# Optimization experiments

Measured on AMD Instinct MI355X. Metric: run time of the kernel, lower is better.

The kernel has to match this reference:

```python
import jax, jax.numpy as jnp
import numpy as np

B, S, D, H = 2, 2048, 1024, 16  # batch, seq, d_model, num_heads
DH = D // H


def setup_inputs() -> dict:
    key = jax.random.key(0)
    ks = jax.random.split(key, 11)
    sc = 1.0 / np.sqrt(D)
    return {
        "q": jax.random.normal(ks[0], (B, S, D), jnp.float32),
        "k": jax.random.normal(ks[1], (B, S, D), jnp.float32),
        "v": jax.random.normal(ks[2], (B, S, D), jnp.float32),
        "wq": jax.random.normal(ks[3], (D, D), jnp.float32) * sc,
        "bq": jax.random.normal(ks[4], (D,), jnp.float32) * 0.01,
        "wk": jax.random.normal(ks[5], (D, D), jnp.float32) * sc,
        "bk": jax.random.normal(ks[6], (D,), jnp.float32) * 0.01,
        "wv": jax.random.normal(ks[7], (D, D), jnp.float32) * sc,
        "bv": jax.random.normal(ks[8], (D,), jnp.float32) * 0.01,
        "wo": jax.random.normal(ks[9], (D, D), jnp.float32) * sc,
        "bo": jax.random.normal(ks[10], (D,), jnp.float32) * 0.01,
    }


def reference(q, k, v, wq, bq, wk, bk, wv, bv, wo, bo):
    # projections: [B,S,D]
    query = q @ wq + bq
    key_ = k @ wk + bk
    value = v @ wv + bv
    # split heads: [B,H,S,DH]
    def split(x):
        return jnp.transpose(x.reshape(B, S, H, DH), (0, 2, 1, 3))
    query, key_, value = split(query), split(key_), split(value)
    # NOTE: original module applies NO 1/sqrt(d_k) scaling
    scores = jnp.einsum("bhqd,bhkd->bhqk", query, key_)
    attn = jax.nn.softmax(scores, axis=-1)
    data = jnp.einsum("bhqk,bhkd->bhqd", attn, value)  # [B,H,S,DH]
    # faithful to original bug: transpose(0,1) then view(B,S,-1)
    data = jnp.swapaxes(data, 0, 1).reshape(B, S, D)
    return data @ wo + bo
```

## Files before the change

### kernel.cpp

```cpp
#include <hip/hip_runtime.h>

typedef _Float16 f16;
typedef _Float16 f16x8 __attribute__((ext_vector_type(8)));
typedef _Float16 f16x4 __attribute__((ext_vector_type(4)));
typedef float    f32x4 __attribute__((ext_vector_type(4)));

static constexpr int BATCH = 2, SEQ = 2048, DMODEL = 1024, HEADS = 16, DHEAD = 64;
static constexpr int MTOK = BATCH * SEQ;
static constexpr float LOG2E = 1.44269504088896f;

#define GLOBAL_LOAD_LDS16(gptr, lptr)                                              \
  __builtin_amdgcn_global_load_lds(                                                \
      (const __attribute__((address_space(1))) void*)(gptr),                       \
      (__attribute__((address_space(3))) void*)(lptr), 16, 0, 0)

#define MFMA16(a, b, c) __builtin_amdgcn_mfma_f32_16x16x32_f16((a), (b), (c), 0, 0, 0)

__device__ __forceinline__ float fexp2(float x) {
  float r;
  asm volatile("v_exp_f32 %0, %1" : "=v"(r) : "v"(x));
  return r;
}

__device__ __forceinline__ int imgAB(int mr, int kr) {
  int pr = mr >> 1;
  int jj = ((mr & 1) << 2) | (kr >> 3);
  int j = jj ^ (pr & 7);
  return pr * 64 + j * 8 + (kr & 7);
}
__device__ __forceinline__ int imgK(int sr, int dh) {
  return sr * 64 + (((dh >> 3) ^ (sr & 7)) << 3) + (dh & 7);
}

__global__ __launch_bounds__(256) void cast_kernel(const float* __restrict__ src,
                                                   f16* __restrict__ dst) {
  int c = blockIdx.x * 256 + threadIdx.x;
  int blk = c >> 8, cb = c & 255;
  int pr = cb >> 3, j = cb & 7;
  int jj = j ^ (pr & 7);
  int mr = (pr << 1) | (jj >> 2);
  int kr = (jj & 3) << 3;
  int m = (blk >> 5) * 64 + mr;
  int k = (blk & 31) * 32 + kr;
  const float* s = src + (size_t)m * DMODEL + k;
  f32x4 a = *(const f32x4*)s, b = *(const f32x4*)(s + 4);
  f16x8 o;
  o[0] = (f16)a[0]; o[1] = (f16)a[1]; o[2] = (f16)a[2]; o[3] = (f16)a[3];
  o[4] = (f16)b[0]; o[5] = (f16)b[1]; o[6] = (f16)b[2]; o[7] = (f16)b[3];
  *(f16x8*)(dst + (size_t)c * 8) = o;
}

__global__ __launch_bounds__(256) void transw_kernel(
    const float* __restrict__ w0, const float* __restrict__ w1,
    const float* __restrict__ w2, const float* __restrict__ w3,
    f16* __restrict__ Wimg) {
  const int z = blockIdx.z;
  const float* w = z == 0 ? w0 : z == 1 ? w1 : z == 2 ? w2 : w3;
  f16* t = Wimg + (size_t)z * DMODEL * DMODEL;
  __shared__ f16 lt[64][72];
  const int k0 = blockIdx.x * 64, n0 = blockIdx.y * 64;
  const int r = threadIdx.x >> 2, c0 = (threadIdx.x & 3) * 16;
  const float* src = w + (size_t)(k0 + r) * DMODEL + n0 + c0;
#pragma unroll
  for (int jx = 0; jx < 16; jx += 4) {
    f32x4 x = *(const f32x4*)(src + jx);
    lt[c0 + jx + 0][r] = (f16)x[0];
    lt[c0 + jx + 1][r] = (f16)x[1];
    lt[c0 + jx + 2][r] = (f16)x[2];
    lt[c0 + jx + 3][r] = (f16)x[3];
  }
  __syncthreads();
  const int n = n0 + r;
#pragma unroll
  for (int cw = 0; cw < 2; cw++) {
    int k = k0 + c0 + cw * 8;
    int blk = ((n >> 6) << 5) | (k >> 5);
    int off = blk * 2048 + imgAB(n & 63, k & 31);
    f16x8 v;
#pragma unroll
    for (int e = 0; e < 8; e++) v[e] = lt[r][c0 + cw * 8 + e];
    *(f16x8*)(t + off) = v;
  }
}

__global__ __launch_bounds__(256) void proj_kernel(
    const f16* __restrict__ Ximg, const f16* __restrict__ Wimg,
    const float* __restrict__ bq, const float* __restrict__ bk,
    const float* __restrict__ bv, f16* __restrict__ Qp, f16* __restrict__ Kp,
    f16* __restrict__ Vt, int zbase, size_t aStride) {
  __shared__ f16 As[4096];
  __shared__ f16 Bs[4096];
  const int z = zbase + blockIdx.z;
  const f16* A = Ximg + (size_t)blockIdx.z * aStride;
  const f16* Bw = Wimg + (size_t)z * DMODEL * DMODEL;
  int lin = blockIdx.x + (blockIdx.y << 3);
  int swz = ((lin & 7) << 5) + (lin >> 3);
  const int n0 = (swz & 7) * 128, m0 = (swz >> 3) * 128;
  const int tid = threadIdx.x, w = tid >> 6, l = tid & 63, q = l & 15, g = l >> 4;
  const int wr = w >> 1, wc = w & 1;
  const int KT = DMODEL >> 5;
  int aoff[4], boff[4];
#pragma unroll
  for (int mi = 0; mi < 4; mi++) {
    int mr = wr * 64 + mi * 16 + q;
    aoff[mi] = ((mr >> 6) << 11) + imgAB(mr & 63, g * 8);
  }
#pragma unroll
  for (int ni = 0; ni < 4; ni++) {
    int nr = wc * 64 + ni * 16 + q;
    boff[ni] = ((nr >> 6) << 11) + imgAB(nr & 63, g * 8);
  }
  f32x4 acc[4][4] = {};
  for (int t = 0; t < KT; t++) {
#pragma unroll
    for (int i = 0; i < 2; i++) {
      int c = w * 2 + i;
      GLOBAL_LOAD_LDS16(A + (size_t)(((m0 >> 6) + (c >> 2)) * KT + t) * 2048 + (c & 3) * 512 + l * 8,
                        (char*)&As[c * 512]);
      GLOBAL_LOAD_LDS16(Bw + (size_t)(((n0 >> 6) + (c >> 2)) * KT + t) * 2048 + (c & 3) * 512 + l * 8,
                        (char*)&Bs[c * 512]);
    }
    __syncthreads();
    f16x8 af[4], bf[4];
#pragma unroll
    for (int mi = 0; mi < 4; mi++) af[mi] = *(const f16x8*)&As[aoff[mi]];
#pragma unroll
    for (int ni = 0; ni < 4; ni++) bf[ni] = *(const f16x8*)&Bs[boff[ni]];
#pragma unroll
    for (int mi = 0; mi < 4; mi++)
#pragma unroll
      for (int ni = 0; ni < 4; ni++)
        acc[mi][ni] = MFMA16(af[mi], bf[ni], acc[mi][ni]);
    __syncthreads();
  }
  const float* bias = z == 0 ? bq : (z == 1 ? bk : bv);
#pragma unroll
  for (int mi = 0; mi < 4; mi++)
#pragma unroll
    for (int ni = 0; ni < 4; ni++) {
      const int col = n0 + wc * 64 + ni * 16 + q;
      const float bvl = bias[col];
      const int row0 = m0 + wr * 64 + mi * 16 + g * 4;
      if (z == 0) {
#pragma unroll
        for (int r = 0; r < 4; r++)
          Qp[(size_t)(row0 + r) * DMODEL + col] = (f16)((acc[mi][ni][r] + bvl) * LOG2E);
      } else if (z == 1) {
        const int h = col >> 6, dh = col & 63;
#pragma unroll
        for (int r = 0; r < 4; r++) {
          const int row = row0 + r, s = row & (SEQ - 1);
          Kp[(size_t)(((row >> 11) * HEADS + h) * 64 + (s >> 5)) * 2048 + imgK(s & 31, dh)] =
              (f16)(acc[mi][ni][r] + bvl);
        }
      } else {
        const int h = col >> 6, dh = col & 63;
        const int s0 = row0 & (SEQ - 1);
        f16* dst = Vt + (size_t)(((row0 >> 11) * HEADS + h) * 64 + (s0 >> 5)) * 2048 +
                   imgAB(dh, s0 & 31);
        f16x4 ov;
        ov[0] = (f16)(acc[mi][ni][0] + bvl); ov[1] = (f16)(acc[mi][ni][1] + bvl);
        ov[2] = (f16)(acc[mi][ni][2] + bvl); ov[3] = (f16)(acc[mi][ni][3] + bvl);
        *(f16x4*)dst = ov;
      }
    }
}

__global__ __launch_bounds__(256) void attn_kernel(
    const f16* __restrict__ Qp, const f16* __restrict__ Kimg,
    const f16* __restrict__ Vimg, f16* __restrict__ Simg) {
  __shared__ f16 Klds[2][2048];
  __shared__ f16 Vlds[2][2048];
  __shared__ f16 Plds[4][512];
  const int tid = threadIdx.x, w = tid >> 6, l = tid & 63, q = l & 15, g = l >> 4;
  int lin = blockIdx.x + (blockIdx.y << 5);
  int swz = ((lin & 7) << 7) + (lin >> 3);
  const int qb = swz & 31, bh = swz >> 5;
  const int b = bh >> 4, h = bh & 15;
  const int q0 = qb * 64 + w * 16;
  const f16* qrow = Qp + (size_t)(b * SEQ + q0 + q) * DMODEL + h * 64;
  const f16x8 qf0 = *(const f16x8*)(qrow + g * 8);
  const f16x8 qf1 = *(const f16x8*)(qrow + 32 + g * 8);
  const f16* kt_base = Kimg + (size_t)(bh * 64) * 2048;
  const f16* vt_base = Vimg + (size_t)(bh * 64) * 2048;
  int koff[2][2];
#pragma unroll
  for (int fn = 0; fn < 2; fn++)
#pragma unroll
    for (int hf = 0; hf < 2; hf++) koff[fn][hf] = imgK(fn * 16 + q, hf * 32 + g * 8);
  int voff[4];
#pragma unroll
  for (int fo = 0; fo < 4; fo++) voff[fo] = imgAB(fo * 16 + q, g * 8);
  const int poff = imgAB(q, g * 8);
  int pwoff[2];
  {
    const int pr = q >> 1;
#pragma unroll
    for (int fn = 0; fn < 2; fn++) {
      int jj = ((q & 1) << 2) | (fn * 2 + (g >> 1));
      pwoff[fn] = pr * 64 + ((jj ^ (pr & 7)) << 3) + (g & 1) * 4;
    }
  }
  f16* Pw = &Plds[w][0];
  float m_st = -1.0e30f, l_pt = 0.f;
  f32x4 o_acc[4] = {};

  GLOBAL_LOAD_LDS16(kt_base + w * 512 + l * 8, (char*)&Klds[0][w * 512]);
  GLOBAL_LOAD_LDS16(vt_base + w * 512 + l * 8, (char*)&Vlds[0][w * 512]);
  __syncthreads();

  for (int t = 0; t < 64; t++) {
    const int bb = t & 1;
    if (t < 63) {
      GLOBAL_LOAD_LDS16(kt_base + (size_t)(t + 1) * 2048 + w * 512 + l * 8,
                        (char*)&Klds[bb ^ 1][w * 512]);
      GLOBAL_LOAD_LDS16(vt_base + (size_t)(t + 1) * 2048 + w * 512 + l * 8,
                        (char*)&Vlds[bb ^ 1][w * 512]);
    }
    const f16* Kb = &Klds[bb][0];
    const f16* Vb = &Vlds[bb][0];
    f32x4 s0 = {}, s1 = {};
    s0 = MFMA16(*(const f16x8*)(Kb + koff[0][0]), qf0, s0);
    s0 = MFMA16(*(const f16x8*)(Kb + koff[0][1]), qf1, s0);
    s1 = MFMA16(*(const f16x8*)(Kb + koff[1][0]), qf0, s1);
    s1 = MFMA16(*(const f16x8*)(Kb + koff[1][1]), qf1, s1);
    float lm = fmaxf(fmaxf(fmaxf(s0[0], s0[1]), fmaxf(s0[2], s0[3])),
                     fmaxf(fmaxf(s1[0], s1[1]), fmaxf(s1[2], s1[3])));
    if (!__all(lm <= m_st + 8.f)) {
      float mx = lm;
      mx = fmaxf(mx, __shfl_xor(mx, 16, 64));
      mx = fmaxf(mx, __shfl_xor(mx, 32, 64));
      const float mnew = fmaxf(m_st, mx);
      const float sc = fexp2(m_st - mnew);
      m_st = mnew;
      l_pt *= sc;
#pragma unroll
      for (int fo = 0; fo < 4; fo++) {
        o_acc[fo][0] *= sc; o_acc[fo][1] *= sc;
        o_acc[fo][2] *= sc; o_acc[fo][3] *= sc;
      }
    }
    f16x4 pa, pb;
    float ts = 0.f;
#pragma unroll
    for (int r = 0; r < 4; r++) {
      float e0 = fexp2(s0[r] - m_st);
      float e1 = fexp2(s1[r] - m_st);
      ts += e0 + e1;
      pa[r] = (f16)e0;
      pb[r] = (f16)e1;
    }
    l_pt += ts;
    *(f16x4*)(Pw + pwoff[0]) = pa;
    *(f16x4*)(Pw + pwoff[1]) = pb;
    const f16x8 pf = *(const f16x8*)(Pw + poff);
#pragma unroll
    for (int fo = 0; fo < 4; fo++)
      o_acc[fo] = MFMA16(*(const f16x8*)(Vb + voff[fo]), pf, o_acc[fo]);
    __syncthreads();
  }
  float lsum = l_pt + __shfl_xor(l_pt, 16, 64);
  lsum += __shfl_xor(lsum, 32, 64);
  const float inv = 1.f / lsum;
  const int s = q0 + q;
  const int m16 = (2 * h + b) & 15, bp = h >> 3;
  const int tp = bp * SEQ + m16 * 128 + (s >> 4);
#pragma unroll
  for (int fo = 0; fo < 4; fo++) {
    const int d0 = (s & 15) * 64 + fo * 16 + g * 4;
    f16* dst = Simg + (size_t)(((tp >> 6) << 5) | (d0 >> 5)) * 2048 + imgAB(tp & 63, d0 & 31);
    f16x4 ov;
    ov[0] = (f16)(o_acc[fo][0] * inv); ov[1] = (f16)(o_acc[fo][1] * inv);
    ov[2] = (f16)(o_acc[fo][2] * inv); ov[3] = (f16)(o_acc[fo][3] * inv);
    *(f16x4*)dst = ov;
  }
}

__global__ __launch_bounds__(256) void ogemm_kernel(
    const f16* __restrict__ Aimg, const f16* __restrict__ Bimg,
    const float* __restrict__ bias, float* __restrict__ out) {
  __shared__ f16 As[4096];
  __shared__ f16 Bs[2048];
  int lin = blockIdx.x + (blockIdx.y << 4);
  int swz = ((lin & 7) << 6) + (lin >> 3);
  const int n0 = (swz & 15) * 64, m0 = (swz >> 4) * 128;
  const int tid = threadIdx.x, w = tid >> 6, l = tid & 63, q = l & 15, g = l >> 4;
  const int wr = w >> 1, wc = w & 1;
  int aoff[4], boff[2];
#pragma unroll
  for (int mi = 0; mi < 4; mi++) {
    int mr = wr * 64 + mi * 16 + q;
    aoff[mi] = ((mr >> 6) << 11) + imgAB(mr & 63, g * 8);
  }
#pragma unroll
  for (int ni = 0; ni < 2; ni++) boff[ni] = imgAB(wc * 32 + ni * 16 + q, g * 8);
  f32x4 acc[4][2] = {};
  for (int t = 0; t < 32; t++) {
#pragma unroll
    for (int i = 0; i < 2; i++) {
      int c = w * 2 + i;
      GLOBAL_LOAD_LDS16(Aimg + (size_t)(((m0 >> 6) + (c >> 2)) * 32 + t) * 2048 + (c & 3) * 512 + l * 8,
                        (char*)&As[c * 512]);
    }
    GLOBAL_LOAD_LDS16(Bimg + ((size_t)(n0 >> 6) * 32 + t) * 2048 + w * 512 + l * 8,
                      (char*)&Bs[w * 512]);
    __syncthreads();
    f16x8 af[4], bf[2];
#pragma unroll
    for (int mi = 0; mi < 4; mi++) af[mi] = *(const f16x8*)&As[aoff[mi]];
#pragma unroll
    for (int ni = 0; ni < 2; ni++) bf[ni] = *(const f16x8*)&Bs[boff[ni]];
#pragma unroll
    for (int mi = 0; mi < 4; mi++)
#pragma unroll
      for (int ni = 0; ni < 2; ni++)
        acc[mi][ni] = MFMA16(af[mi], bf[ni], acc[mi][ni]);
    __syncthreads();
  }
#pragma unroll
  for (int mi = 0; mi < 4; mi++)
#pragma unroll
    for (int ni = 0; ni < 2; ni++) {
      const int col = n0 + wc * 32 + ni * 16 + q;
      const float bvl = bias[col];
      const int row0 = m0 + wr * 64 + mi * 16 + g * 4;
#pragma unroll
      for (int r = 0; r < 4; r++)
        out[(size_t)(row0 + r) * DMODEL + col] = acc[mi][ni][r] + bvl;
    }
}

extern "C" void kernel_launch(void* const* d_in, const int* in_sizes, int n_in,
                              void* d_out, int out_size, void* d_ws, size_t ws_size,
                              hipStream_t stream) {
  const float* q  = (const float*)d_in[0];
  const float* k  = (const float*)d_in[1];
  const float* v  = (const float*)d_in[2];
  const float* wq = (const float*)d_in[3];
  const float* bq = (const float*)d_in[4];
  const float* wk = (const float*)d_in[5];
  const float* bk = (const float*)d_in[6];
  const float* wv = (const float*)d_in[7];
  const float* bv = (const float*)d_in[8];
  const float* wo = (const float*)d_in[9];
  const float* bo = (const float*)d_in[10];

  const size_t XSZ = (size_t)MTOK * DMODEL;
  f16* ws = (f16*)d_ws;
  const bool fused = ws_size >= (56ull << 20);

  f16 *X0, *X1, *X2, *Qp, *Kp, *Vt, *Wimg, *scr;
  if (fused) {
    X0 = ws; X1 = ws + XSZ; X2 = ws + 2 * XSZ;
    Qp = ws + 3 * XSZ; Kp = ws + 4 * XSZ; Vt = ws + 5 * XSZ;
    Wimg = ws + 6 * XSZ;
    scr = X0;
  } else {
    X0 = X1 = X2 = ws;
    Qp = ws + XSZ; Kp = ws + 2 * XSZ; Vt = ws + 3 * XSZ;
    Wimg = ws + 4 * XSZ;
    scr = X0;
  }

  dim3 blk(256);
  dim3 gT(16, 16, 4);
  dim3 gC(2048);
  dim3 gA(32, 32);
  dim3 gO(16, 32);

  transw_kernel<<<gT, blk, 0, stream>>>(wq, wk, wv, wo, Wimg);

  if (fused) {
    cast_kernel<<<gC, blk, 0, stream>>>(q, X0);
    cast_kernel<<<gC, blk, 0, stream>>>(k, X1);
    cast_kernel<<<gC, blk, 0, stream>>>(v, X2);
    proj_kernel<<<dim3(8, 32, 3), blk, 0, stream>>>(X0, Wimg, bq, bk, bv, Qp, Kp, Vt, 0, XSZ);
  } else {
    cast_kernel<<<gC, blk, 0, stream>>>(q, X0);
    proj_kernel<<<dim3(8, 32, 1), blk, 0, stream>>>(X0, Wimg, bq, bk, bv, Qp, Kp, Vt, 0, 0);
    cast_kernel<<<gC, blk, 0, stream>>>(k, X0);
    proj_kernel<<<dim3(8, 32, 1), blk, 0, stream>>>(X0, Wimg, bq, bk, bv, Qp, Kp, Vt, 1, 0);
    cast_kernel<<<gC, blk, 0, stream>>>(v, X0);
    proj_kernel<<<dim3(8, 32, 1), blk, 0, stream>>>(X0, Wimg, bq, bk, bv, Qp, Kp, Vt, 2, 0);
  }

  attn_kernel<<<gA, blk, 0, stream>>>(Qp, Kp, Vt, scr);
  ogemm_kernel<<<gO, blk, 0, stream>>>(scr, Wimg + (size_t)3 * DMODEL * DMODEL, bo, (float*)d_out);
}
```

Measured before the change: 247.2 us.

## Rewrite attention as single-wave blocks with register K/V and deepen GEMM K-tiles

The attention kernel becomes one 64-thread wave per block. Each wave handles two 16-row query tiles and loads K and V fragments straight from global memory into registers, double-buffered. This drops the LDS staging and block-wide barriers, and K/V are reused across both query tiles. K and V are now stored in plain row-major and transposed layouts, and the projection and output GEMMs process 64-wide K steps per barrier, halving the sync count at the cost of larger LDS tiles. The risks are uncoalesced strided V loads and higher register pressure from holding two K/V buffers.

```diff
diff --git a/kernel.cpp b/kernel.cpp
--- a/kernel.cpp
+++ b/kernel.cpp
@@ -27,9 +27,6 @@
   int jj = ((mr & 1) << 2) | (kr >> 3);
   int j = jj ^ (pr & 7);
   return pr * 64 + j * 8 + (kr & 7);
-}
-__device__ __forceinline__ int imgK(int sr, int dh) {
-  return sr * 64 + (((dh >> 3) ^ (sr & 7)) << 3) + (dh & 7);
 }
 
 __global__ __launch_bounds__(256) void cast_kernel(const float* __restrict__ src,
@@ -88,8 +85,8 @@
     const float* __restrict__ bq, const float* __restrict__ bk,
     const float* __restrict__ bv, f16* __restrict__ Qp, f16* __restrict__ Kp,
     f16* __restrict__ Vt, int zbase, size_t aStride) {
-  __shared__ f16 As[4096];
-  __shared__ f16 Bs[4096];
+  __shared__ f16 As[8192];
+  __shared__ f16 Bs[8192];
   const int z = zbase + blockIdx.z;
   const f16* A = Ximg + (size_t)blockIdx.z * aStride;
   const f16* Bw = Wimg + (size_t)z * DMODEL * DMODEL;
@@ -98,39 +95,51 @@
   const int n0 = (swz & 7) * 128, m0 = (swz >> 3) * 128;
   const int tid = threadIdx.x, w = tid >> 6, l = tid & 63, q = l & 15, g = l >> 4;
   const int wr = w >> 1, wc = w & 1;
-  const int KT = DMODEL >> 5;
-  int aoff[4], boff[4];
+  int aoff[4][2], boff[4][2];
 #pragma unroll
   for (int mi = 0; mi < 4; mi++) {
     int mr = wr * 64 + mi * 16 + q;
-    aoff[mi] = ((mr >> 6) << 11) + imgAB(mr & 63, g * 8);
+#pragma unroll
+    for (int kb = 0; kb < 2; kb++)
+      aoff[mi][kb] = (((mr >> 6) << 1) | kb) * 2048 + imgAB(mr & 63, g * 8);
   }
 #pragma unroll
   for (int ni = 0; ni < 4; ni++) {
     int nr = wc * 64 + ni * 16 + q;
-    boff[ni] = ((nr >> 6) << 11) + imgAB(nr & 63, g * 8);
+#pragma unroll
+    for (int kb = 0; kb < 2; kb++)
+      boff[ni][kb] = (((nr >> 6) << 1) | kb) * 2048 + imgAB(nr & 63, g * 8);
   }
   f32x4 acc[4][4] = {};
-  for (int t = 0; t < KT; t++) {
-#pragma unroll
-    for (int i = 0; i < 2; i++) {
-      int c = w * 2 + i;
-      GLOBAL_LOAD_LDS16(A + (size_t)(((m0 >> 6) + (c >> 2)) * KT + t) * 2048 + (c & 3) * 512 + l * 8,
-                        (char*)&As[c * 512]);
-      GLOBAL_LOAD_LDS16(Bw + (size_t)(((n0 >> 6) + (c >> 2)) * KT + t) * 2048 + (c & 3) * 512 + l * 8,
-                        (char*)&Bs[c * 512]);
+  for (int t = 0; t < 16; t++) {
+#pragma unroll
+    for (int i = 0; i < 4; i++) {
+      int c = w * 4 + i;
+      int bi = c >> 2, part = c & 3;
+      size_t gblk = (size_t)(((m0 >> 6) + (bi >> 1)) * 32 + t * 2 + (bi & 1));
+      GLOBAL_LOAD_LDS16(A + gblk * 2048 + part * 512 + l * 8, (char*)&As[c * 512]);
+      size_t gblk2 = (size_t)(((n0 >> 6) + (bi >> 1)) * 32 + t * 2 + (bi & 1));
+      GLOBAL_LOAD_LDS16(Bw + gblk2 * 2048 + part * 512 + l * 8, (char*)&Bs[c * 512]);
     }
     __syncthreads();
-    f16x8 af[4], bf[4];
-#pragma unroll
-    for (int mi = 0; mi < 4; mi++) af[mi] = *(const f16x8*)&As[aoff[mi]];
-#pragma unroll
-    for (int ni = 0; ni < 4; ni++) bf[ni] = *(const f16x8*)&Bs[boff[ni]];
+    f16x8 af[4][2], bf[4][2];
+#pragma unroll
+    for (int mi = 0; mi < 4; mi++) {
+      af[mi][0] = *(const f16x8*)&As[aoff[mi][0]];
+      af[mi][1] = *(const f16x8*)&As[aoff[mi][1]];
+    }
+#pragma unroll
+    for (int ni = 0; ni < 4; ni++) {
+      bf[ni][0] = *(const f16x8*)&Bs[boff[ni][0]];
+      bf[ni][1] = *(const f16x8*)&Bs[boff[ni][1]];
+    }
 #pragma unroll
     for (int mi = 0; mi < 4; mi++)
 #pragma unroll
-      for (int ni = 0; ni < 4; ni++)
-        acc[mi][ni] = MFMA16(af[mi], bf[ni], acc[mi][ni]);
+      for (int ni = 0; ni < 4; ni++) {
+        acc[mi][ni] = MFMA16(af[mi][0], bf[ni][0], acc[mi][ni]);
+        acc[mi][ni] = MFMA16(af[mi][1], bf[ni][1], acc[mi][ni]);
+      }
     __syncthreads();
   }
   const float* bias = z == 0 ? bq : (z == 1 ? bk : bv);
@@ -146,18 +155,13 @@
         for (int r = 0; r < 4; r++)
           Qp[(size_t)(row0 + r) * DMODEL + col] = (f16)((acc[mi][ni][r] + bvl) * LOG2E);
       } else if (z == 1) {
-        const int h = col >> 6, dh = col & 63;
-#pragma unroll
-        for (int r = 0; r < 4; r++) {
-          const int row = row0 + r, s = row & (SEQ - 1);
-          Kp[(size_t)(((row >> 11) * HEADS + h) * 64 + (s >> 5)) * 2048 + imgK(s & 31, dh)] =
-              (f16)(acc[mi][ni][r] + bvl);
-        }
+#pragma unroll
+        for (int r = 0; r < 4; r++)
+          Kp[(size_t)(row0 + r) * DMODEL + col] = (f16)(acc[mi][ni][r] + bvl);
       } else {
         const int h = col >> 6, dh = col & 63;
-        const int s0 = row0 & (SEQ - 1);
-        f16* dst = Vt + (size_t)(((row0 >> 11) * HEADS + h) * 64 + (s0 >> 5)) * 2048 +
-                   imgAB(dh, s0 & 31);
+        const int b2 = row0 >> 11, s0 = row0 & (SEQ - 1);
+        f16* dst = Vt + ((size_t)(b2 * HEADS + h) * DHEAD + dh) * SEQ + s0;
         f16x4 ov;
         ov[0] = (f16)(acc[mi][ni][0] + bvl); ov[1] = (f16)(acc[mi][ni][1] + bvl);
         ov[2] = (f16)(acc[mi][ni][2] + bvl); ov[3] = (f16)(acc[mi][ni][3] + bvl);
@@ -166,32 +170,30 @@
     }
 }
 
-__global__ __launch_bounds__(256) void attn_kernel(
-    const f16* __restrict__ Qp, const f16* __restrict__ Kimg,
-    const f16* __restrict__ Vimg, f16* __restrict__ Simg) {
-  __shared__ f16 Klds[2][2048];
-  __shared__ f16 Vlds[2][2048];
-  __shared__ f16 Plds[4][512];
-  const int tid = threadIdx.x, w = tid >> 6, l = tid & 63, q = l & 15, g = l >> 4;
-  int lin = blockIdx.x + (blockIdx.y << 5);
-  int swz = ((lin & 7) << 7) + (lin >> 3);
-  const int qb = swz & 31, bh = swz >> 5;
+__global__ __launch_bounds__(64, 2) void attn_kernel(
+    const f16* __restrict__ Qp, const f16* __restrict__ Kp,
+    const f16* __restrict__ Vt, f16* __restrict__ Simg) {
+  __shared__ f16 Plds[1024];
+  const int l = threadIdx.x, q = l & 15, g = l >> 4;
+  const int bid = blockIdx.x;
+  const int gid = (bid & 7) * 256 + (bid >> 3);
+  const int bh = gid >> 6, qt = gid & 63;
   const int b = bh >> 4, h = bh & 15;
-  const int q0 = qb * 64 + w * 16;
-  const f16* qrow = Qp + (size_t)(b * SEQ + q0 + q) * DMODEL + h * 64;
-  const f16x8 qf0 = *(const f16x8*)(qrow + g * 8);
-  const f16x8 qf1 = *(const f16x8*)(qrow + 32 + g * 8);
-  const f16* kt_base = Kimg + (size_t)(bh * 64) * 2048;
-  const f16* vt_base = Vimg + (size_t)(bh * 64) * 2048;
-  int koff[2][2];
-#pragma unroll
-  for (int fn = 0; fn < 2; fn++)
-#pragma unroll
-    for (int hf = 0; hf < 2; hf++) koff[fn][hf] = imgK(fn * 16 + q, hf * 32 + g * 8);
-  int voff[4];
-#pragma unroll
-  for (int fo = 0; fo < 4; fo++) voff[fo] = imgAB(fo * 16 + q, g * 8);
-  const int poff = imgAB(q, g * 8);
+  const int q0 = qt * 32;
+
+  const f16* qra = Qp + (size_t)(b * SEQ + q0 + q) * DMODEL + h * 64;
+  const f16x8 qa0 = *(const f16x8*)(qra + g * 8);
+  const f16x8 qa1 = *(const f16x8*)(qra + 32 + g * 8);
+  const f16* qrb = qra + (size_t)16 * DMODEL;
+  const f16x8 qb0 = *(const f16x8*)(qrb + g * 8);
+  const f16x8 qb1 = *(const f16x8*)(qrb + 32 + g * 8);
+
+  const f16* kp = Kp + ((size_t)b * SEQ + q) * DMODEL + h * 64 + g * 8;
+  const f16* vp = Vt + ((size_t)bh * DHEAD + q) * SEQ + g * 8;
+
+  float mA = -1.0e30f, mB = -1.0e30f, lA = 0.f, lB = 0.f;
+  f32x4 oA[4] = {}, oB[4] = {};
+
   int pwoff[2];
   {
     const int pr = q >> 1;
@@ -201,120 +203,168 @@
       pwoff[fn] = pr * 64 + ((jj ^ (pr & 7)) << 3) + (g & 1) * 4;
     }
   }
-  f16* Pw = &Plds[w][0];
-  float m_st = -1.0e30f, l_pt = 0.f;
-  f32x4 o_acc[4] = {};
-
-  GLOBAL_LOAD_LDS16(kt_base + w * 512 + l * 8, (char*)&Klds[0][w * 512]);
-  GLOBAL_LOAD_LDS16(vt_base + w * 512 + l * 8, (char*)&Vlds[0][w * 512]);
-  __syncthreads();
-
-  for (int t = 0; t < 64; t++) {
-    const int bb = t & 1;
-    if (t < 63) {
-      GLOBAL_LOAD_LDS16(kt_base + (size_t)(t + 1) * 2048 + w * 512 + l * 8,
-                        (char*)&Klds[bb ^ 1][w * 512]);
-      GLOBAL_LOAD_LDS16(vt_base + (size_t)(t + 1) * 2048 + w * 512 + l * 8,
-                        (char*)&Vlds[bb ^ 1][w * 512]);
-    }
-    const f16* Kb = &Klds[bb][0];
-    const f16* Vb = &Vlds[bb][0];
-    f32x4 s0 = {}, s1 = {};
-    s0 = MFMA16(*(const f16x8*)(Kb + koff[0][0]), qf0, s0);
-    s0 = MFMA16(*(const f16x8*)(Kb + koff[0][1]), qf1, s0);
-    s1 = MFMA16(*(const f16x8*)(Kb + koff[1][0]), qf0, s1);
-    s1 = MFMA16(*(const f16x8*)(Kb + koff[1][1]), qf1, s1);
-    float lm = fmaxf(fmaxf(fmaxf(s0[0], s0[1]), fmaxf(s0[2], s0[3])),
-                     fmaxf(fmaxf(s1[0], s1[1]), fmaxf(s1[2], s1[3])));
-    if (!__all(lm <= m_st + 8.f)) {
-      float mx = lm;
-      mx = fmaxf(mx, __shfl_xor(mx, 16, 64));
-      mx = fmaxf(mx, __shfl_xor(mx, 32, 64));
-      const float mnew = fmaxf(m_st, mx);
-      const float sc = fexp2(m_st - mnew);
-      m_st = mnew;
-      l_pt *= sc;
-#pragma unroll
-      for (int fo = 0; fo < 4; fo++) {
-        o_acc[fo][0] *= sc; o_acc[fo][1] *= sc;
-        o_acc[fo][2] *= sc; o_acc[fo][3] *= sc;
-      }
-    }
-    f16x4 pa, pb;
-    float ts = 0.f;
-#pragma unroll
-    for (int r = 0; r < 4; r++) {
-      float e0 = fexp2(s0[r] - m_st);
-      float e1 = fexp2(s1[r] - m_st);
-      ts += e0 + e1;
-      pa[r] = (f16)e0;
-      pb[r] = (f16)e1;
-    }
-    l_pt += ts;
-    *(f16x4*)(Pw + pwoff[0]) = pa;
-    *(f16x4*)(Pw + pwoff[1]) = pb;
-    const f16x8 pf = *(const f16x8*)(Pw + poff);
-#pragma unroll
-    for (int fo = 0; fo < 4; fo++)
-      o_acc[fo] = MFMA16(*(const f16x8*)(Vb + voff[fo]), pf, o_acc[fo]);
-    __syncthreads();
-  }
-  float lsum = l_pt + __shfl_xor(l_pt, 16, 64);
-  lsum += __shfl_xor(lsum, 32, 64);
-  const float inv = 1.f / lsum;
-  const int s = q0 + q;
+  const int poff = imgAB(q, g * 8);
+
+  f16x8 Ak0, Ak1, Ak2, Ak3, Av0, Av1, Av2, Av3;
+  f16x8 Bk0, Bk1, Bk2, Bk3, Bv0, Bv1, Bv2, Bv3;
+
+#define LOADKV(S, t)                                                               \
+  {                                                                                \
+    const f16* kk_ = kp + (size_t)(t) * (32 * DMODEL);                             \
+    S##k0 = *(const f16x8*)(kk_);                                                  \
+    S##k1 = *(const f16x8*)(kk_ + 32);                                             \
+    S##k2 = *(const f16x8*)(kk_ + 16 * DMODEL);                                    \
+    S##k3 = *(const f16x8*)(kk_ + 16 * DMODEL + 32);                               \
+    const f16* vv_ = vp + (t) * 32;                                                \
+    S##v0 = *(const f16x8*)(vv_);                                                  \
+    S##v1 = *(const f16x8*)(vv_ + 16 * SEQ);                                       \
+    S##v2 = *(const f16x8*)(vv_ + 32 * SEQ);                                       \
+    S##v3 = *(const f16x8*)(vv_ + 48 * SEQ);                                       \
+  }
+
+#define SOFTMAX_FRAG(s0, s1, m, lsum, o, pk0, pk1)                                 \
+  {                                                                                \
+    float lm = fmaxf(fmaxf(fmaxf(s0[0], s0[1]), fmaxf(s0[2], s0[3])),              \
+                     fmaxf(fmaxf(s1[0], s1[1]), fmaxf(s1[2], s1[3])));             \
+    if (!__all(lm <= m + 8.f)) {                                                   \
+      float mx = fmaxf(lm, __shfl_xor(lm, 16, 64));                                \
+      mx = fmaxf(mx, __shfl_xor(mx, 32, 64));                                      \
+      const float mnew = fmaxf(m, mx);                                             \
+      const float sc = fexp2(m - mnew);                                            \
+      m = mnew;                                                                    \
+      lsum *= sc;                                                                  \
+      _Pragma("unroll")                                                            \
+      for (int fo_ = 0; fo_ < 4; fo_++) {                                          \
+        o[fo_][0] *= sc; o[fo_][1] *= sc; o[fo_][2] *= sc; o[fo_][3] *= sc;        \
+      }                                                                            \
+    }                                                                              \
+    float ts = 0.f;                                                                \
+    _Pragma("unroll")                                                              \
+    for (int r_ = 0; r_ < 4; r_++) {                                               \
+      float e0 = fexp2(s0[r_] - m);                                                \
+      float e1 = fexp2(s1[r_] - m);                                                \
+      ts += e0 + e1;                                                               \
+      pk0[r_] = (f16)e0;                                                           \
+      pk1[r_] = (f16)e1;                                                           \
+    }                                                                              \
+    lsum += ts;                                                                    \
+  }
+
+#define COMPUTE(S)                                                                 \
+  {                                                                                \
+    f32x4 sA0 = {}, sA1 = {}, sB0 = {}, sB1 = {};                                  \
+    sA0 = MFMA16(S##k0, qa0, sA0); sA0 = MFMA16(S##k1, qa1, sA0);                  \
+    sA1 = MFMA16(S##k2, qa0, sA1); sA1 = MFMA16(S##k3, qa1, sA1);                  \
+    sB0 = MFMA16(S##k0, qb0, sB0); sB0 = MFMA16(S##k1, qb1, sB0);                  \
+    sB1 = MFMA16(S##k2, qb0, sB1); sB1 = MFMA16(S##k3, qb1, sB1);                  \
+    f16x4 pa0, pa1, pb0, pb1;                                                      \
+    SOFTMAX_FRAG(sA0, sA1, mA, lA, oA, pa0, pa1);                                  \
+    SOFTMAX_FRAG(sB0, sB1, mB, lB, oB, pb0, pb1);                                  \
+    *(f16x4*)(&Plds[0] + pwoff[0]) = pa0;                                          \
+    *(f16x4*)(&Plds[0] + pwoff[1]) = pa1;                                          \
+    *(f16x4*)(&Plds[512] + pwoff[0]) = pb0;                                        \
+    *(f16x4*)(&Plds[512] + pwoff[1]) = pb1;                                        \
+    const f16x8 pfA = *(const f16x8*)(&Plds[0] + poff);                            \
+    const f16x8 pfB = *(const f16x8*)(&Plds[512] + poff);                          \
+    oA[0] = MFMA16(S##v0, pfA, oA[0]); oB[0] = MFMA16(S##v0, pfB, oB[0]);          \
+    oA[1] = MFMA16(S##v1, pfA, oA[1]); oB[1] = MFMA16(S##v1, pfB, oB[1]);          \
+    oA[2] = MFMA16(S##v2, pfA, oA[2]); oB[2] = MFMA16(S##v2, pfB, oB[2]);          \
+    oA[3] = MFMA16(S##v3, pfA, oA[3]); oB[3] = MFMA16(S##v3, pfB, oB[3]);          \
+  }
+
+  LOADKV(A, 0);
+  LOADKV(B, 1);
+  for (int t = 0; t < 64; t += 2) {
+    COMPUTE(A);
+    if (t + 2 < 64) LOADKV(A, t + 2);
+    COMPUTE(B);
+    if (t + 3 < 64) LOADKV(B, t + 3);
+  }
+
+  float lsA = lA + __shfl_xor(lA, 16, 64);
+  lsA += __shfl_xor(lsA, 32, 64);
+  float lsB = lB + __shfl_xor(lB, 16, 64);
+  lsB += __shfl_xor(lsB, 32, 64);
+  const float invA = 1.f / lsA, invB = 1.f / lsB;
   const int m16 = (2 * h + b) & 15, bp = h >> 3;
-  const int tp = bp * SEQ + m16 * 128 + (s >> 4);
-#pragma unroll
-  for (int fo = 0; fo < 4; fo++) {
-    const int d0 = (s & 15) * 64 + fo * 16 + g * 4;
-    f16* dst = Simg + (size_t)(((tp >> 6) << 5) | (d0 >> 5)) * 2048 + imgAB(tp & 63, d0 & 31);
-    f16x4 ov;
-    ov[0] = (f16)(o_acc[fo][0] * inv); ov[1] = (f16)(o_acc[fo][1] * inv);
-    ov[2] = (f16)(o_acc[fo][2] * inv); ov[3] = (f16)(o_acc[fo][3] * inv);
-    *(f16x4*)dst = ov;
+#pragma unroll
+  for (int half = 0; half < 2; half++) {
+    const int s = q0 + half * 16 + q;
+    const int tp = bp * SEQ + m16 * 128 + (s >> 4);
+    const float inv = half ? invB : invA;
+    const f32x4* o = half ? oB : oA;
+#pragma unroll
+    for (int fo = 0; fo < 4; fo++) {
+      const int d0 = (s & 15) * 64 + fo * 16 + g * 4;
+      f16* dst = Simg + (size_t)(((tp >> 6) << 5) | (d0 >> 5)) * 2048 + imgAB(tp & 63, d0 & 31);
+      f16x4 ov;
+      ov[0] = (f16)(o[fo][0] * inv); ov[1] = (f16)(o[fo][1] * inv);
+      ov[2] = (f16)(o[fo][2] * inv); ov[3] = (f16)(o[fo][3] * inv);
+      *(f16x4*)dst = ov;
+    }
   }
 }
 
 __global__ __launch_bounds__(256) void ogemm_kernel(
     const f16* __restrict__ Aimg, const f16* __restrict__ Bimg,
     const float* __restrict__ bias, float* __restrict__ out) {
-  __shared__ f16 As[4096];
-  __shared__ f16 Bs[2048];
+  __shared__ f16 As[8192];
+  __shared__ f16 Bs[4096];
   int lin = blockIdx.x + (blockIdx.y << 4);
   int swz = ((lin & 7) << 6) + (lin >> 3);
   const int n0 = (swz & 15) * 64, m0 = (swz >> 4) * 128;
   const int tid = threadIdx.x, w = tid >> 6, l = tid & 63, q = l & 15, g = l >> 4;
   const int wr = w >> 1, wc = w & 1;
-  int aoff[4], boff[2];
+  int aoff[4][2], boff[2][2];
 #pragma unroll
   for (int mi = 0; mi < 4; mi++) {
     int mr = wr * 64 + mi * 16 + q;
-    aoff[mi] = ((mr >> 6) << 11) + imgAB(mr & 63, g * 8);
-  }
-#pragma unroll
-  for (int ni = 0; ni < 2; ni++) boff[ni] = imgAB(wc * 32 + ni * 16 + q, g * 8);
+#pragma unroll
+    for (int kb = 0; kb < 2; kb++)
+      aoff[mi][kb] = (((mr >> 6) << 1) | kb) * 2048 + imgAB(mr & 63, g * 8);
+  }
+#pragma unroll
+  for (int ni = 0; ni < 2; ni++) {
+    int nr = wc * 32 + ni * 16 + q;
+#pragma unroll
+    for (int kb = 0; kb < 2; kb++)
+      boff[ni][kb] = kb * 2048 + imgAB(nr & 63, g * 8);
+  }
   f32x4 acc[4][2] = {};
-  for (int t = 0; t < 32; t++) {
+  for (int t = 0; t < 16; t++) {
+#pragma unroll
+    for (int i = 0; i < 4; i++) {
+      int c = w * 4 + i;
+      int bi = c >> 2, part = c & 3;
+      size_t gblk = (size_t)(((m0 >> 6) + (bi >> 1)) * 32 + t * 2 + (bi & 1));
+      GLOBAL_LOAD_LDS16(Aimg + gblk * 2048 + part * 512 + l * 8, (char*)&As[c * 512]);
+    }
 #pragma unroll
     for (int i = 0; i < 2; i++) {
       int c = w * 2 + i;
-      GLOBAL_LOAD_LDS16(Aimg + (size_t)(((m0 >> 6) + (c >> 2)) * 32 + t) * 2048 + (c & 3) * 512 + l * 8,
-                        (char*)&As[c * 512]);
-    }
-    GLOBAL_LOAD_LDS16(Bimg + ((size_t)(n0 >> 6) * 32 + t) * 2048 + w * 512 + l * 8,
-                      (char*)&Bs[w * 512]);
+      int bi = c >> 2, part = c & 3;
+      size_t gblk = (size_t)((n0 >> 6) * 32 + t * 2 + (bi & 1));
+      GLOBAL_LOAD_LDS16(Bimg + gblk * 2048 + part * 512 + l * 8, (char*)&Bs[c * 512]);
+    }
     __syncthreads();
-    f16x8 af[4], bf[2];
-#pragma unroll
-    for (int mi = 0; mi < 4; mi++) af[mi] = *(const f16x8*)&As[aoff[mi]];
-#pragma unroll
-    for (int ni = 0; ni < 2; ni++) bf[ni] = *(const f16x8*)&Bs[boff[ni]];
+    f16x8 af[4][2], bf[2][2];
+#pragma unroll
+    for (int mi = 0; mi < 4; mi++) {
+      af[mi][0] = *(const f16x8*)&As[aoff[mi][0]];
+      af[mi][1] = *(const f16x8*)&As[aoff[mi][1]];
+    }
+#pragma unroll
+    for (int ni = 0; ni < 2; ni++) {
+      bf[ni][0] = *(const f16x8*)&Bs[boff[ni][0]];
+      bf[ni][1] = *(const f16x8*)&Bs[boff[ni][1]];
+    }
 #pragma unroll
     for (int mi = 0; mi < 4; mi++)
 #pragma unroll
-      for (int ni = 0; ni < 2; ni++)
-        acc[mi][ni] = MFMA16(af[mi], bf[ni], acc[mi][ni]);
+      for (int ni = 0; ni < 2; ni++) {
+        acc[mi][ni] = MFMA16(af[mi][0], bf[ni][0], acc[mi][ni]);
+        acc[mi][ni] = MFMA16(af[mi][1], bf[ni][1], acc[mi][ni]);
+      }
     __syncthreads();
   }
 #pragma unroll
@@ -365,7 +415,7 @@
   dim3 blk(256);
   dim3 gT(16, 16, 4);
   dim3 gC(2048);
-  dim3 gA(32, 32);
+  dim3 gA(2048);
   dim3 gO(16, 32);
 
   transw_kernel<<<gT, blk, 0, stream>>>(wq, wk, wv, wo, Wimg);
@@ -384,6 +434,6 @@
     proj_kernel<<<dim3(8, 32, 1), blk, 0, stream>>>(X0, Wimg, bq, bk, bv, Qp, Kp, Vt, 2, 0);
   }
 
-  attn_kernel<<<gA, blk, 0, stream>>>(Qp, Kp, Vt, scr);
+  attn_kernel<<<gA, dim3(64), 0, stream>>>(Qp, Kp, Vt, scr);
   ogemm_kernel<<<gO, blk, 0, stream>>>(scr, Wimg + (size_t)3 * DMODEL * DMODEL, bo, (float*)d_out);
 }
```

Result: slower. 303.1 us (+22.6%).
